# Performance work log

Hardware: AMD Instinct MI355X
Metric: run time of the kernel (lower is better)

The kernel has to match this reference:

```python
import jax, jax.numpy as jnp
import numpy as np

B, N, E, H = 128, 1024, 512, 8
DK = E // H
TANH_CLIP = 10.0


def setup_inputs() -> dict:
    key = jax.random.key(0)
    k0, k1, k2, k3, k4, k5 = jax.random.split(key, 6)
    query = jax.random.normal(k0, (B, 1, E), dtype=jnp.float32)
    glimpse_K = jax.random.normal(k1, (H, B, 1, N, DK), dtype=jnp.float32)
    glimpse_V = jax.random.normal(k2, (H, B, 1, N, DK), dtype=jnp.float32)
    logit_K = jax.random.normal(k3, (B, 1, N, E), dtype=jnp.float32)
    W_out = jax.random.normal(k4, (E, E), dtype=jnp.float32) / np.float32(np.sqrt(E))
    mask = jax.random.bernoulli(k5, 0.3, (B, 1, N))  # True = infeasible
    return {"query": query, "glimpse_K": glimpse_K, "glimpse_V": glimpse_V,
            "logit_K": logit_K, "W_out": W_out, "mask": mask}


def reference(query, glimpse_K, glimpse_V, logit_K, W_out, mask):
    # query: [B,S=1,E]; glimpse_K/V: [H,B,S,N,DK]; logit_K: [B,S,N,E]; mask: [B,S,N]
    h, b, s, n, dk = glimpse_K.shape
    e = query.shape[-1]
    neg_inf = jnp.float32(-jnp.inf)

    # glimpse_Q: view [B,S,H,1,DK] -> permute -> [H,B,S,1,DK]
    glimpse_Q = query.reshape(b, s, h, 1, dk).transpose(2, 0, 1, 3, 4)

    # compatibility: [H,B,S,1,N]
    compat = jnp.einsum('hbsqd,hbsnd->hbsqn', glimpse_Q, glimpse_K) / jnp.sqrt(jnp.float32(dk))
    compat = jnp.where(mask[None, :, :, None, :], neg_inf, compat)  # mask_inner

    attn = jax.nn.softmax(compat, axis=-1)
    heads = jnp.einsum('hbsqn,hbsnd->hbsqd', attn, glimpse_V)  # [H,B,S,1,DK]

    # permute(1,2,3,0,4).view(B,S,1,H*DK) then project_out (Linear, no bias -> x @ W^T)
    glimpse = heads.transpose(1, 2, 3, 0, 4).reshape(b, s, 1, h * dk) @ W_out.T  # [B,S,1,E]

    # logits: [B,S,1,N] -> squeeze(-2) -> [B,S,N]
    logits = jnp.einsum('bsqe,bsne->bsqn', glimpse, logit_K)[:, :, 0, :] / jnp.sqrt(jnp.float32(e))
    logits = jnp.tanh(logits) * jnp.float32(TANH_CLIP)
    logits = jnp.where(mask, neg_inf, logits)  # mask_logits

    return logits, glimpse[:, :, 0, :]  # ([B,S,N], [B,S,E])
```

## Files before the change

kernel.cpp:

```cpp
#include <hip/hip_runtime.h>
#include <hip/hip_bf16.h>
#include <math.h>

#define B_ 128
#define N_ 1024
#define E_ 512
#define H_ 8
#define DK_ 64

#define NEG_BIG (-1.0e30f)

typedef float f32x4 __attribute__((ext_vector_type(4)));

__device__ __forceinline__ float dot4v(f32x4 a, f32x4 b) {
    return a[0] * b[0] + a[1] * b[1] + a[2] * b[2] + a[3] * b[3];
}

__device__ __forceinline__ f32x4 ntload4(const float* p) {
    return __builtin_nontemporal_load(reinterpret_cast<const f32x4*>(p));
}

__device__ __forceinline__ bool mask_at(const void* mask, int isByte, int idx) {
    return isByte ? (((const unsigned char*)mask)[idx] != 0)
                  : (((const int*)mask)[idx] != 0);
}

__device__ __forceinline__ int detect_byte_mask(const void* mask, int lane) {
    unsigned w = ((const unsigned*)mask)[lane];
    return (__ballot(w > 1u) != 0ull) ? 1 : 0;
}

__global__ __launch_bounds__(512, 8) void attn_heads_kernel(
    const float* __restrict__ query,
    const float* __restrict__ gK,
    const float* __restrict__ gV,
    const void*  __restrict__ mask,
    float* __restrict__ hcat)
{
    const int blk  = blockIdx.x;
    const int h    = blk >> 7;
    const int b    = blk & 127;
    const int tid  = threadIdx.x;
    const int wave = tid >> 6;
    const int lane = tid & 63;
    const int p    = lane & 15;
    const int r    = lane >> 4;
    const int isByte = detect_byte_mask(mask, lane);
    const int bN   = b * N_;

    __shared__ float s[N_];
    __shared__ float redmax[8];
    __shared__ float redsum[8];
    __shared__ float part[8][64];

    const f32x4 q4 = *reinterpret_cast<const f32x4*>(
        query + (size_t)b * E_ + h * DK_ + p * 4);

    const float* Kp = gK + (size_t)blk * N_ * DK_;
    const float* Vp = gV + (size_t)blk * N_ * DK_;

    const int base = wave * 4 + r;
    float wmax = -INFINITY;
    for (int n0 = base; n0 < N_; n0 += 128) {
        const int nA = n0, nB = n0 + 32, nC = n0 + 64, nD = n0 + 96;
        const bool lA = !mask_at(mask, isByte, bN + nA);
        const bool lB = !mask_at(mask, isByte, bN + nB);
        const bool lC = !mask_at(mask, isByte, bN + nC);
        const bool lD = !mask_at(mask, isByte, bN + nD);
        f32x4 kA = {0.f,0.f,0.f,0.f}, kB = {0.f,0.f,0.f,0.f};
        f32x4 kC = {0.f,0.f,0.f,0.f}, kD = {0.f,0.f,0.f,0.f};
        if (lA) kA = ntload4(Kp + nA * DK_ + p * 4);
        if (lB) kB = ntload4(Kp + nB * DK_ + p * 4);
        if (lC) kC = ntload4(Kp + nC * DK_ + p * 4);
        if (lD) kD = ntload4(Kp + nD * DK_ + p * 4);
        float vA = dot4v(q4, kA), vB = dot4v(q4, kB);
        float vC = dot4v(q4, kC), vD = dot4v(q4, kD);
        vA += __shfl_xor(vA, 1); vB += __shfl_xor(vB, 1);
        vC += __shfl_xor(vC, 1); vD += __shfl_xor(vD, 1);
        vA += __shfl_xor(vA, 2); vB += __shfl_xor(vB, 2);
        vC += __shfl_xor(vC, 2); vD += __shfl_xor(vD, 2);
        vA += __shfl_xor(vA, 4); vB += __shfl_xor(vB, 4);
        vC += __shfl_xor(vC, 4); vD += __shfl_xor(vD, 4);
        vA += __shfl_xor(vA, 8); vB += __shfl_xor(vB, 8);
        vC += __shfl_xor(vC, 8); vD += __shfl_xor(vD, 8);
        vA *= 0.125f; vB *= 0.125f; vC *= 0.125f; vD *= 0.125f;
        wmax = fmaxf(fmaxf(wmax, fmaxf(vA, vB)), fmaxf(vC, vD));
        if (p == 0) {
            s[nA] = lA ? vA : -INFINITY;
            s[nB] = lB ? vB : -INFINITY;
            s[nC] = lC ? vC : -INFINITY;
            s[nD] = lD ? vD : -INFINITY;
        }
    }
    wmax = fmaxf(wmax, __shfl_xor(wmax, 16));
    wmax = fmaxf(wmax, __shfl_xor(wmax, 32));
    if (lane == 0) redmax[wave] = wmax;
    __syncthreads();
    float bmax = redmax[0];
    #pragma unroll
    for (int i = 1; i < 8; ++i) bmax = fmaxf(bmax, redmax[i]);

    float lsum = 0.f;
    #pragma unroll
    for (int k = 0; k < N_ / 512; ++k) {
        const int n = tid + k * 512;
        float e = __expf(s[n] - bmax);
        s[n] = e;
        lsum += e;
    }
    lsum += __shfl_xor(lsum, 1);
    lsum += __shfl_xor(lsum, 2);
    lsum += __shfl_xor(lsum, 4);
    lsum += __shfl_xor(lsum, 8);
    lsum += __shfl_xor(lsum, 16);
    lsum += __shfl_xor(lsum, 32);
    if (lane == 0) redsum[wave] = lsum;
    __syncthreads();
    float bsum = redsum[0];
    #pragma unroll
    for (int i = 1; i < 8; ++i) bsum += redsum[i];
    const float invsum = 1.0f / bsum;

    f32x4 acc = {0.f, 0.f, 0.f, 0.f};
    for (int n0 = base; n0 < N_; n0 += 128) {
        const int nA = n0, nB = n0 + 32, nC = n0 + 64, nD = n0 + 96;
        const float wA = s[nA], wB = s[nB], wC = s[nC], wD = s[nD];
        f32x4 a4 = {0.f,0.f,0.f,0.f}, b4 = {0.f,0.f,0.f,0.f};
        f32x4 c4 = {0.f,0.f,0.f,0.f}, d4 = {0.f,0.f,0.f,0.f};
        if (wA != 0.f) a4 = ntload4(Vp + nA * DK_ + p * 4);
        if (wB != 0.f) b4 = ntload4(Vp + nB * DK_ + p * 4);
        if (wC != 0.f) c4 = ntload4(Vp + nC * DK_ + p * 4);
        if (wD != 0.f) d4 = ntload4(Vp + nD * DK_ + p * 4);
        acc += wA * a4 + wB * b4 + wC * c4 + wD * d4;
    }
    acc[0] += __shfl_xor(acc[0], 16); acc[0] += __shfl_xor(acc[0], 32);
    acc[1] += __shfl_xor(acc[1], 16); acc[1] += __shfl_xor(acc[1], 32);
    acc[2] += __shfl_xor(acc[2], 16); acc[2] += __shfl_xor(acc[2], 32);
    acc[3] += __shfl_xor(acc[3], 16); acc[3] += __shfl_xor(acc[3], 32);
    if (r == 0) {
        part[wave][p * 4 + 0] = acc[0];
        part[wave][p * 4 + 1] = acc[1];
        part[wave][p * 4 + 2] = acc[2];
        part[wave][p * 4 + 3] = acc[3];
    }
    __syncthreads();
    if (tid < 64) {
        float sum = 0.f;
        #pragma unroll
        for (int w = 0; w < 8; ++w) sum += part[w][tid];
        hcat[(size_t)b * E_ + h * DK_ + tid] = sum * invsum;
    }
}

__global__ __launch_bounds__(256) void proj_kernel(
    const float* __restrict__ hcat,
    const float* __restrict__ W_out,
    float* __restrict__ glimpse)
{
    const int b     = blockIdx.x >> 2;
    const int chunk = blockIdx.x & 3;
    const int tid   = threadIdx.x;
    const int wave  = tid >> 6;
    const int lane  = tid & 63;

    __shared__ f32x4 h4[E_ / 4];
    if (tid < E_ / 4)
        h4[tid] = reinterpret_cast<const f32x4*>(hcat + (size_t)b * E_)[tid];
    __syncthreads();

    const f32x4* W4 = reinterpret_cast<const f32x4*>(W_out);
    const int e_begin = chunk * 128;
    for (int e = e_begin + wave; e < e_begin + 128; e += 4) {
        const f32x4* row = W4 + (size_t)e * (E_ / 4);
        float v = dot4v(h4[lane], row[lane]) + dot4v(h4[64 + lane], row[64 + lane]);
        v += __shfl_xor(v, 1);
        v += __shfl_xor(v, 2);
        v += __shfl_xor(v, 4);
        v += __shfl_xor(v, 8);
        v += __shfl_xor(v, 16);
        v += __shfl_xor(v, 32);
        if (lane == 0) glimpse[(size_t)b * E_ + e] = v;
    }
}

__global__ __launch_bounds__(512, 8) void logits_kernel(
    const float* __restrict__ glimpse,
    const float* __restrict__ logit_K,
    const void*  __restrict__ mask,
    float* __restrict__ logits)
{
    const int b     = blockIdx.x >> 3;
    const int chunk = blockIdx.x & 7;
    const int tid   = threadIdx.x;
    const int wave  = tid >> 6;
    const int lane  = tid & 63;
    const int isByte = detect_byte_mask(mask, lane);

    __shared__ f32x4 g4[E_ / 4];
    if (tid < E_ / 4)
        g4[tid] = reinterpret_cast<const f32x4*>(glimpse + (size_t)b * E_)[tid];
    __syncthreads();

    const float inv_sqrt_e = 0.04419417382415922f;
    const f32x4* LK4 = reinterpret_cast<const f32x4*>(logit_K);
    const int n_begin = chunk * 128;

    #define FTANH(x) (1.0f - 2.0f / (__expf(2.0f * (x)) + 1.0f))

    for (int j = 0; j < 16; j += 4) {
        const int nA = n_begin + wave + 8 * j;
        const int nB = nA + 8, nC = nA + 16, nD = nA + 24;
        const bool mA = mask_at(mask, isByte, b * N_ + nA);
        const bool mB = mask_at(mask, isByte, b * N_ + nB);
        const bool mC = mask_at(mask, isByte, b * N_ + nC);
        const bool mD = mask_at(mask, isByte, b * N_ + nD);
        f32x4 a0 = {0.f,0.f,0.f,0.f}, a1 = {0.f,0.f,0.f,0.f};
        f32x4 b0 = {0.f,0.f,0.f,0.f}, b1 = {0.f,0.f,0.f,0.f};
        f32x4 c0 = {0.f,0.f,0.f,0.f}, c1 = {0.f,0.f,0.f,0.f};
        f32x4 d0 = {0.f,0.f,0.f,0.f}, d1 = {0.f,0.f,0.f,0.f};
        const f32x4* rowA = LK4 + ((size_t)b * N_ + nA) * (E_ / 4);
        const f32x4* rowB = LK4 + ((size_t)b * N_ + nB) * (E_ / 4);
        const f32x4* rowC = LK4 + ((size_t)b * N_ + nC) * (E_ / 4);
        const f32x4* rowD = LK4 + ((size_t)b * N_ + nD) * (E_ / 4);
        if (!mA) { a0 = rowA[lane]; a1 = rowA[64 + lane]; }
        if (!mB) { b0 = rowB[lane]; b1 = rowB[64 + lane]; }
        if (!mC) { c0 = rowC[lane]; c1 = rowC[64 + lane]; }
        if (!mD) { d0 = rowD[lane]; d1 = rowD[64 + lane]; }
        float vA = dot4v(g4[lane], a0) + dot4v(g4[64 + lane], a1);
        float vB = dot4v(g4[lane], b0) + dot4v(g4[64 + lane], b1);
        float vC = dot4v(g4[lane], c0) + dot4v(g4[64 + lane], c1);
        float vD = dot4v(g4[lane], d0) + dot4v(g4[64 + lane], d1);
        vA += __shfl_xor(vA, 1);  vB += __shfl_xor(vB, 1);
        vC += __shfl_xor(vC, 1);  vD += __shfl_xor(vD, 1);
        vA += __shfl_xor(vA, 2);  vB += __shfl_xor(vB, 2);
        vC += __shfl_xor(vC, 2);  vD += __shfl_xor(vD, 2);
        vA += __shfl_xor(vA, 4);  vB += __shfl_xor(vB, 4);
        vC += __shfl_xor(vC, 4);  vD += __shfl_xor(vD, 4);
        vA += __shfl_xor(vA, 8);  vB += __shfl_xor(vB, 8);
        vC += __shfl_xor(vC, 8);  vD += __shfl_xor(vD, 8);
        vA += __shfl_xor(vA, 16); vB += __shfl_xor(vB, 16);
        vC += __shfl_xor(vC, 16); vD += __shfl_xor(vD, 16);
        vA += __shfl_xor(vA, 32); vB += __shfl_xor(vB, 32);
        vC += __shfl_xor(vC, 32); vD += __shfl_xor(vD, 32);
        if (lane == 0) {
            logits[(size_t)b * N_ + nA] = mA ? NEG_BIG : FTANH(vA * inv_sqrt_e) * 10.0f;
            logits[(size_t)b * N_ + nB] = mB ? NEG_BIG : FTANH(vB * inv_sqrt_e) * 10.0f;
            logits[(size_t)b * N_ + nC] = mC ? NEG_BIG : FTANH(vC * inv_sqrt_e) * 10.0f;
            logits[(size_t)b * N_ + nD] = mD ? NEG_BIG : FTANH(vD * inv_sqrt_e) * 10.0f;
        }
    }
    #undef FTANH
}

extern "C" void kernel_launch(void* const* d_in, const int* in_sizes, int n_in,
                              void* d_out, int out_size, void* d_ws, size_t ws_size,
                              hipStream_t stream) {
    const float* query   = (const float*)d_in[0];
    const float* gK      = (const float*)d_in[1];
    const float* gV      = (const float*)d_in[2];
    const float* logit_K = (const float*)d_in[3];
    const float* W_out   = (const float*)d_in[4];
    const void*  mask    = (const void*)d_in[5];

    float* logits_out  = (float*)d_out;
    float* glimpse_out = (float*)d_out + (size_t)B_ * N_;
    float* hcat        = (float*)d_ws;

    attn_heads_kernel<<<dim3(H_ * B_), dim3(512), 0, stream>>>(
        query, gK, gV, mask, hcat);
    proj_kernel<<<dim3(B_ * 4), dim3(256), 0, stream>>>(
        hcat, W_out, glimpse_out);
    logits_kernel<<<dim3(B_ * 8), dim3(512), 0, stream>>>(
        glimpse_out, logit_K, mask, logits_out);
}
```

Baseline: 111.5 us.

## Fuse glimpse QK and PV passes with online softmax per row group

Replaces the two-pass attention (scores to shared memory, block-wide max and sum, then a second sweep over V) with a single pass. Each row group keeps a running max, sum and accumulator (online softmax), and the groups are merged with one final rescale. K and V for the same keys are loaded together, which removes a pass over the score buffer and two block barriers and lets V loads overlap K loads. In exchange it adds per-iteration exps for rescaling, uses more registers, and changes the floating-point summation order.

```diff
diff --git a/kernel.cpp b/kernel.cpp
--- a/kernel.cpp
+++ b/kernel.cpp
@@ -48,9 +48,8 @@
     const int isByte = detect_byte_mask(mask, lane);
     const int bN   = b * N_;
 
-    __shared__ float s[N_];
-    __shared__ float redmax[8];
-    __shared__ float redsum[8];
+    __shared__ float smM[32];
+    __shared__ float smL[8];
     __shared__ float part[8][64];
 
     const f32x4 q4 = *reinterpret_cast<const f32x4*>(
@@ -60,95 +59,86 @@
     const float* Vp = gV + (size_t)blk * N_ * DK_;
 
     const int base = wave * 4 + r;
-    float wmax = -INFINITY;
+    float m = -INFINITY;
+    float l = 0.f;
+    f32x4 acc = {0.f, 0.f, 0.f, 0.f};
+
     for (int n0 = base; n0 < N_; n0 += 128) {
         const int nA = n0, nB = n0 + 32, nC = n0 + 64, nD = n0 + 96;
-        const bool lA = !mask_at(mask, isByte, bN + nA);
-        const bool lB = !mask_at(mask, isByte, bN + nB);
-        const bool lC = !mask_at(mask, isByte, bN + nC);
-        const bool lD = !mask_at(mask, isByte, bN + nD);
+        const bool mA = mask_at(mask, isByte, bN + nA);
+        const bool mB = mask_at(mask, isByte, bN + nB);
+        const bool mC = mask_at(mask, isByte, bN + nC);
+        const bool mD = mask_at(mask, isByte, bN + nD);
         f32x4 kA = {0.f,0.f,0.f,0.f}, kB = {0.f,0.f,0.f,0.f};
         f32x4 kC = {0.f,0.f,0.f,0.f}, kD = {0.f,0.f,0.f,0.f};
-        if (lA) kA = ntload4(Kp + nA * DK_ + p * 4);
-        if (lB) kB = ntload4(Kp + nB * DK_ + p * 4);
-        if (lC) kC = ntload4(Kp + nC * DK_ + p * 4);
-        if (lD) kD = ntload4(Kp + nD * DK_ + p * 4);
-        float vA = dot4v(q4, kA), vB = dot4v(q4, kB);
-        float vC = dot4v(q4, kC), vD = dot4v(q4, kD);
-        vA += __shfl_xor(vA, 1); vB += __shfl_xor(vB, 1);
-        vC += __shfl_xor(vC, 1); vD += __shfl_xor(vD, 1);
-        vA += __shfl_xor(vA, 2); vB += __shfl_xor(vB, 2);
-        vC += __shfl_xor(vC, 2); vD += __shfl_xor(vD, 2);
-        vA += __shfl_xor(vA, 4); vB += __shfl_xor(vB, 4);
-        vC += __shfl_xor(vC, 4); vD += __shfl_xor(vD, 4);
-        vA += __shfl_xor(vA, 8); vB += __shfl_xor(vB, 8);
-        vC += __shfl_xor(vC, 8); vD += __shfl_xor(vD, 8);
-        vA *= 0.125f; vB *= 0.125f; vC *= 0.125f; vD *= 0.125f;
-        wmax = fmaxf(fmaxf(wmax, fmaxf(vA, vB)), fmaxf(vC, vD));
-        if (p == 0) {
-            s[nA] = lA ? vA : -INFINITY;
-            s[nB] = lB ? vB : -INFINITY;
-            s[nC] = lC ? vC : -INFINITY;
-            s[nD] = lD ? vD : -INFINITY;
+        f32x4 vA4 = {0.f,0.f,0.f,0.f}, vB4 = {0.f,0.f,0.f,0.f};
+        f32x4 vC4 = {0.f,0.f,0.f,0.f}, vD4 = {0.f,0.f,0.f,0.f};
+        if (!mA) kA = ntload4(Kp + nA * DK_ + p * 4);
+        if (!mB) kB = ntload4(Kp + nB * DK_ + p * 4);
+        if (!mC) kC = ntload4(Kp + nC * DK_ + p * 4);
+        if (!mD) kD = ntload4(Kp + nD * DK_ + p * 4);
+        if (!mA) vA4 = ntload4(Vp + nA * DK_ + p * 4);
+        if (!mB) vB4 = ntload4(Vp + nB * DK_ + p * 4);
+        if (!mC) vC4 = ntload4(Vp + nC * DK_ + p * 4);
+        if (!mD) vD4 = ntload4(Vp + nD * DK_ + p * 4);
+
+        float sA = dot4v(q4, kA), sB = dot4v(q4, kB);
+        float sC = dot4v(q4, kC), sD = dot4v(q4, kD);
+        sA += __shfl_xor(sA, 1); sB += __shfl_xor(sB, 1);
+        sC += __shfl_xor(sC, 1); sD += __shfl_xor(sD, 1);
+        sA += __shfl_xor(sA, 2); sB += __shfl_xor(sB, 2);
+        sC += __shfl_xor(sC, 2); sD += __shfl_xor(sD, 2);
+        sA += __shfl_xor(sA, 4); sB += __shfl_xor(sB, 4);
+        sC += __shfl_xor(sC, 4); sD += __shfl_xor(sD, 4);
+        sA += __shfl_xor(sA, 8); sB += __shfl_xor(sB, 8);
+        sC += __shfl_xor(sC, 8); sD += __shfl_xor(sD, 8);
+        sA = mA ? -INFINITY : sA * 0.125f;
+        sB = mB ? -INFINITY : sB * 0.125f;
+        sC = mC ? -INFINITY : sC * 0.125f;
+        sD = mD ? -INFINITY : sD * 0.125f;
+
+        const float bm = fmaxf(fmaxf(sA, sB), fmaxf(sC, sD));
+        const float m_new = fmaxf(m, bm);
+        if (m_new != -INFINITY) {
+            const float scale = __expf(m - m_new);
+            l *= scale;
+            acc *= scale;
+            const float wA = mA ? 0.f : __expf(sA - m_new);
+            const float wB = mB ? 0.f : __expf(sB - m_new);
+            const float wC = mC ? 0.f : __expf(sC - m_new);
+            const float wD = mD ? 0.f : __expf(sD - m_new);
+            l += wA + wB + wC + wD;
+            acc += wA * vA4 + wB * vB4 + wC * vC4 + wD * vD4;
+            m = m_new;
         }
     }
-    wmax = fmaxf(wmax, __shfl_xor(wmax, 16));
-    wmax = fmaxf(wmax, __shfl_xor(wmax, 32));
-    if (lane == 0) redmax[wave] = wmax;
-    __syncthreads();
-    float bmax = redmax[0];
+
+    if (p == 0) smM[base] = m;
+    __syncthreads();
+    float M = smM[0];
     #pragma unroll
-    for (int i = 1; i < 8; ++i) bmax = fmaxf(bmax, redmax[i]);
-
-    float lsum = 0.f;
-    #pragma unroll
-    for (int k = 0; k < N_ / 512; ++k) {
-        const int n = tid + k * 512;
-        float e = __expf(s[n] - bmax);
-        s[n] = e;
-        lsum += e;
-    }
-    lsum += __shfl_xor(lsum, 1);
-    lsum += __shfl_xor(lsum, 2);
-    lsum += __shfl_xor(lsum, 4);
-    lsum += __shfl_xor(lsum, 8);
-    lsum += __shfl_xor(lsum, 16);
-    lsum += __shfl_xor(lsum, 32);
-    if (lane == 0) redsum[wave] = lsum;
-    __syncthreads();
-    float bsum = redsum[0];
-    #pragma unroll
-    for (int i = 1; i < 8; ++i) bsum += redsum[i];
-    const float invsum = 1.0f / bsum;
-
-    f32x4 acc = {0.f, 0.f, 0.f, 0.f};
-    for (int n0 = base; n0 < N_; n0 += 128) {
-        const int nA = n0, nB = n0 + 32, nC = n0 + 64, nD = n0 + 96;
-        const float wA = s[nA], wB = s[nB], wC = s[nC], wD = s[nD];
-        f32x4 a4 = {0.f,0.f,0.f,0.f}, b4 = {0.f,0.f,0.f,0.f};
-        f32x4 c4 = {0.f,0.f,0.f,0.f}, d4 = {0.f,0.f,0.f,0.f};
-        if (wA != 0.f) a4 = ntload4(Vp + nA * DK_ + p * 4);
-        if (wB != 0.f) b4 = ntload4(Vp + nB * DK_ + p * 4);
-        if (wC != 0.f) c4 = ntload4(Vp + nC * DK_ + p * 4);
-        if (wD != 0.f) d4 = ntload4(Vp + nD * DK_ + p * 4);
-        acc += wA * a4 + wB * b4 + wC * c4 + wD * d4;
-    }
+    for (int i = 1; i < 32; ++i) M = fmaxf(M, smM[i]);
+    const float f = (m == -INFINITY) ? 0.f : __expf(m - M);
+    acc *= f;
+    float lf = l * f;
     acc[0] += __shfl_xor(acc[0], 16); acc[0] += __shfl_xor(acc[0], 32);
     acc[1] += __shfl_xor(acc[1], 16); acc[1] += __shfl_xor(acc[1], 32);
     acc[2] += __shfl_xor(acc[2], 16); acc[2] += __shfl_xor(acc[2], 32);
     acc[3] += __shfl_xor(acc[3], 16); acc[3] += __shfl_xor(acc[3], 32);
+    lf += __shfl_xor(lf, 16); lf += __shfl_xor(lf, 32);
     if (r == 0) {
         part[wave][p * 4 + 0] = acc[0];
         part[wave][p * 4 + 1] = acc[1];
         part[wave][p * 4 + 2] = acc[2];
         part[wave][p * 4 + 3] = acc[3];
     }
+    if (lane == 0) smL[wave] = lf;
     __syncthreads();
     if (tid < 64) {
-        float sum = 0.f;
+        float sum = 0.f, L = 0.f;
         #pragma unroll
-        for (int w = 0; w < 8; ++w) sum += part[w][tid];
-        hcat[(size_t)b * E_ + h * DK_ + tid] = sum * invsum;
+        for (int w = 0; w < 8; ++w) { sum += part[w][tid]; L += smL[w]; }
+        hcat[(size_t)b * E_ + h * DK_ + tid] = sum / L;
     }
 }
 
```

New measurement: 144.5 us. 1.3x slower.
